# Kernel tuning notes

Measured on AMD Instinct MI355X. Metric: run time of the kernel, lower is better.

## Reference

```python
import jax, jax.numpy as jnp
import numpy as np
import math

SCALES = [1, 2, 4, 8]
H = 1024           # hidden_size
NS = len(SCALES)
DS = H // NS       # per-scale dim = 256
NH_S = max(1, 8 // NS)  # heads per scale = 2


def _avg_pool(x, s):
    # x: [B, L, d], kernel=stride=s (L divisible by s)
    B, L, d = x.shape
    return x.reshape(B, L // s, s, d).mean(axis=2)


def _mha(q, k, v, in_w, in_b, out_w, out_b, nh):
    # torch nn.MultiheadAttention, batch_first, no mask.
    d = q.shape[-1]
    wq, wk, wv = in_w[:d], in_w[d:2 * d], in_w[2 * d:]
    bq, bk, bv = in_b[:d], in_b[d:2 * d], in_b[2 * d:]
    qh = q @ wq.T + bq
    kh = k @ wk.T + bk
    vh = v @ wv.T + bv
    B, Lq, _ = qh.shape
    Lk = kh.shape[1]
    hd = d // nh
    qh = qh.reshape(B, Lq, nh, hd).transpose(0, 2, 1, 3)
    kh = kh.reshape(B, Lk, nh, hd).transpose(0, 2, 1, 3)
    vh = vh.reshape(B, Lk, nh, hd).transpose(0, 2, 1, 3)
    scores = jnp.einsum('bhqd,bhkd->bhqk', qh, kh) * (1.0 / math.sqrt(hd))
    w = jax.nn.softmax(scores, axis=-1)
    out = jnp.einsum('bhqk,bhkd->bhqd', w, vh)
    out = out.transpose(0, 2, 1, 3).reshape(B, Lq, d)
    out = out @ out_w.T + out_b
    return out, w.mean(axis=1)  # averaged attn weights (torch default)


def setup_inputs() -> dict:
    key = jax.random.key(0)
    ks = jax.random.split(key, 20)
    B, S = 4, 2048
    f = lambda k, shape: (jax.random.normal(k, shape, dtype=jnp.float32) * 0.02)
    return {
        'query': jax.random.normal(ks[0], (B, S, H), dtype=jnp.float32),
        'key': jax.random.normal(ks[1], (B, S, H), dtype=jnp.float32),
        'value': jax.random.normal(ks[2], (B, S, H), dtype=jnp.float32),
        'wq': f(ks[3], (H, H)), 'bq': f(ks[4], (H,)),
        'wk': f(ks[5], (H, H)), 'bk': f(ks[6], (H,)),
        'wv': f(ks[7], (H, H)), 'bv': f(ks[8], (H,)),
        'mha_in_w': f(ks[9], (NS, 3 * DS, DS)),
        'mha_in_b': f(ks[10], (NS, 3 * DS)),
        'mha_out_w': f(ks[11], (NS, DS, DS)),
        'mha_out_b': f(ks[12], (NS, DS)),
        'fus_w': f(ks[13], (H, H)), 'fus_b': f(ks[14], (H,)),
    }


def reference(query, key, value, wq, bq, wk, bk, wv, bv,
              mha_in_w, mha_in_b, mha_out_w, mha_out_b, fus_w, fus_b):
    q = query @ wq.T + bq
    k = key @ wk.T + bk
    v = value @ wv.T + bv
    outs = []
    weights0 = None
    for i, s in enumerate(SCALES):
        qs = q[..., i * DS:(i + 1) * DS]
        ks_ = k[..., i * DS:(i + 1) * DS]
        vs = v[..., i * DS:(i + 1) * DS]
        if s > 1:
            ks_ = _avg_pool(ks_, s)
            vs = _avg_pool(vs, s)
        attended, w = _mha(qs, ks_, vs, mha_in_w[i], mha_in_b[i],
                           mha_out_w[i], mha_out_b[i], NH_S)
        # F.interpolate back to seq_len is an identity here (query length == seq_len)
        outs.append(attended)
        if i == 0:
            weights0 = w
    fused = jnp.concatenate(outs, axis=-1) @ fus_w.T + fus_b
    return fused, weights0
```

## Files before the change

### kernel.cpp

```cpp
#include <hip/hip_runtime.h>
#include <stdint.h>

typedef unsigned short u16;
typedef __bf16 v8bf __attribute__((ext_vector_type(8)));
typedef float v4f __attribute__((ext_vector_type(4)));
typedef __attribute__((address_space(3))) unsigned lds_t;
typedef const __attribute__((address_space(1))) unsigned g_t;

__device__ __forceinline__ u16 f2bf(float f) {
  union { float f; unsigned u; } v; v.f = f;
  unsigned r = v.u + 0x7FFFu + ((v.u >> 16) & 1u);
  return (u16)(r >> 16);
}
__device__ __forceinline__ float bf2f(u16 h) {
  union { unsigned u; float f; } v; v.u = ((unsigned)h) << 16;
  return v.f;
}
__device__ __forceinline__ ushort4 f4bf(float4 f) {
  ushort4 o;
  o.x = f2bf(f.x); o.y = f2bf(f.y); o.z = f2bf(f.z); o.w = f2bf(f.w);
  return o;
}
__device__ __forceinline__ long sel4(long4 v, int z) {
  return z == 0 ? v.x : z == 1 ? v.y : z == 2 ? v.z : v.w;
}
__device__ __forceinline__ int sel4i(int4 v, int z) {
  return z == 0 ? v.x : z == 1 ? v.y : z == 2 ? v.z : v.w;
}

__global__ void k_cvt(const float* __restrict__ s, u16* __restrict__ d, long n) {
  long i = ((long)blockIdx.x * blockDim.x + threadIdx.x) * 4;
  long stride = (long)gridDim.x * blockDim.x * 4;
  for (; i < n; i += stride) {
    *(ushort4*)(d + i) = f4bf(*(const float4*)(s + i));
  }
}

__global__ void k_cvtpool(const float* __restrict__ src, u16* __restrict__ dst) {
  int g = blockIdx.x & 255, b = blockIdx.x >> 8;
  int c = threadIdx.x * 4;
  const float* p = src + ((long)b * 2048 + g * 8) * 1024 + c;
  u16* df = dst + ((long)b * 2048 + g * 8) * 1024 + c;
  float4 x[8];
#pragma unroll
  for (int j = 0; j < 8; j++) {
    x[j] = *(const float4*)(p + (long)j * 1024);
    *(ushort4*)(df + (long)j * 1024) = f4bf(x[j]);
  }
  float4 s2[4], s4[2], s8;
#pragma unroll
  for (int j = 0; j < 4; j++) {
    s2[j].x = x[2 * j].x + x[2 * j + 1].x;
    s2[j].y = x[2 * j].y + x[2 * j + 1].y;
    s2[j].z = x[2 * j].z + x[2 * j + 1].z;
    s2[j].w = x[2 * j].w + x[2 * j + 1].w;
  }
#pragma unroll
  for (int j = 0; j < 2; j++) {
    s4[j].x = s2[2 * j].x + s2[2 * j + 1].x;
    s4[j].y = s2[2 * j].y + s2[2 * j + 1].y;
    s4[j].z = s2[2 * j].z + s2[2 * j + 1].z;
    s4[j].w = s2[2 * j].w + s2[2 * j + 1].w;
  }
  s8.x = s4[0].x + s4[1].x; s8.y = s4[0].y + s4[1].y;
  s8.z = s4[0].z + s4[1].z; s8.w = s4[0].w + s4[1].w;
  u16* d2 = dst + ((long)8192 + b * 1024 + g * 4) * 1024 + c;
#pragma unroll
  for (int j = 0; j < 4; j++) {
    float4 t = {s2[j].x * 0.5f, s2[j].y * 0.5f, s2[j].z * 0.5f, s2[j].w * 0.5f};
    *(ushort4*)(d2 + (long)j * 1024) = f4bf(t);
  }
  u16* d4 = dst + ((long)12288 + b * 512 + g * 2) * 1024 + c;
#pragma unroll
  for (int j = 0; j < 2; j++) {
    float4 t = {s4[j].x * 0.25f, s4[j].y * 0.25f, s4[j].z * 0.25f, s4[j].w * 0.25f};
    *(ushort4*)(d4 + (long)j * 1024) = f4bf(t);
  }
  float4 t8 = {s8.x * 0.125f, s8.y * 0.125f, s8.z * 0.125f, s8.w * 0.125f};
  *(ushort4*)(dst + ((long)14336 + b * 256 + g) * 1024 + c) = f4bf(t8);
}

__global__ void k_tc(const float* __restrict__ src, u16* __restrict__ dst, int R, int C) {
  __shared__ float t[32][33];
  long zoff = (long)blockIdx.z * R * C;
  int r0 = blockIdx.y * 32, c0 = blockIdx.x * 32;
  int tx = threadIdx.x & 31, ty = threadIdx.x >> 5;
#pragma unroll
  for (int j = 0; j < 32; j += 8)
    t[ty + j][tx] = src[zoff + (long)(r0 + ty + j) * C + c0 + tx];
  __syncthreads();
#pragma unroll
  for (int j = 0; j < 32; j += 8)
    dst[zoff + (long)(c0 + ty + j) * R + r0 + tx] = f2bf(t[tx][ty + j]);
}

__global__ void k_bcomb_qkv(const float* __restrict__ in_w, const float* __restrict__ in_b,
                            const float* __restrict__ bq, const float* __restrict__ bk,
                            const float* __restrict__ bv, float* __restrict__ out) {
  int gw = (blockIdx.x * 256 + threadIdx.x) >> 6;
  int lane = threadIdx.x & 63;
  int p = gw >> 10, j = gw & 1023, i = j >> 8, of = j & 255;
  const float* bp = p == 0 ? bq : p == 1 ? bk : bv;
  const float* row = in_w + ((long)i * 768 + p * 256 + of) * 256;
  float s = 0.f;
#pragma unroll
  for (int m = 0; m < 4; m++) s += row[lane + m * 64] * bp[i * 256 + lane + m * 64];
#pragma unroll
  for (int m = 32; m >= 1; m >>= 1) s += __shfl_xor(s, m, 64);
  if (lane == 0) out[gw] = in_b[(long)i * 768 + p * 256 + of] + s;
}

__global__ void k_bcomb_f(const float* __restrict__ fw, const float* __restrict__ fb,
                          const float* __restrict__ ob, float* __restrict__ out) {
  int w = (blockIdx.x * 256 + threadIdx.x) >> 6;
  int lane = threadIdx.x & 63;
  const float* row = fw + (long)w * 1024;
  float s = 0.f;
  for (int k = lane; k < 1024; k += 64) s += row[k] * ob[k];
#pragma unroll
  for (int m = 32; m >= 1; m >>= 1) s += __shfl_xor(s, m, 64);
  if (lane == 0) out[w] = fb[w] + s;
}

template<int KS>
__global__ __launch_bounds__(256) void k_ksum(const float* __restrict__ P,
                                              u16* __restrict__ O, long n, int coloff) {
  long i = ((long)blockIdx.x * 256 + threadIdx.x) * 4;
  if (i >= n) return;
  float4 s = *(const float4*)(P + i);
#pragma unroll
  for (int ks = 1; ks < KS; ks++) {
    float4 t = *(const float4*)(P + (long)ks * n + i);
    s.x += t.x; s.y += t.y; s.z += t.z; s.w += t.w;
  }
  *(ushort4*)(O + (i >> 8) * 1024 + coloff + (int)(i & 255)) = f4bf(s);
}

__device__ __forceinline__ float block_allreduce(float x, bool domax) {
  __shared__ float t[4];
  int lane = threadIdx.x & 63, w = threadIdx.x >> 6;
#pragma unroll
  for (int m = 32; m >= 1; m >>= 1) {
    float o = __shfl_xor(x, m, 64);
    x = domax ? fmaxf(x, o) : (x + o);
  }
  __syncthreads();
  if (lane == 0) t[w] = x;
  __syncthreads();
  return domax ? fmaxf(fmaxf(t[0], t[1]), fmaxf(t[2], t[3]))
               : (t[0] + t[1] + t[2] + t[3]);
}

template<int LK>
__global__ __launch_bounds__(256) void k_softmax(u16* __restrict__ P) {
  constexpr int E = LK / 256;
  long row = blockIdx.x;
  u16* p = P + row * (long)LK;
  int tid = threadIdx.x;
  float v[E];
  float mx = -1e30f;
#pragma unroll
  for (int i = 0; i < E; i++) { v[i] = bf2f(p[tid + i * 256]); mx = fmaxf(mx, v[i]); }
  mx = block_allreduce(mx, true);
  float s = 0.f;
#pragma unroll
  for (int i = 0; i < E; i++) { v[i] = __expf(v[i] - mx); s += v[i]; }
  s = block_allreduce(s, false);
  float inv = 1.0f / s;
#pragma unroll
  for (int i = 0; i < E; i++) p[tid + i * 256] = f2bf(v[i] * inv);
}

__global__ __launch_bounds__(256) void k_softmax0(u16* __restrict__ P, float* __restrict__ W0) {
  int bq = blockIdx.x;
  int b = bq >> 11, q = bq & 2047;
  int tid = threadIdx.x;
  float pw[2][8];
  for (int h = 0; h < 2; h++) {
    u16* p = P + (((long)(b * 2 + h) * 2048 + q) * 2048);
    float v[8];
    float mx = -1e30f;
#pragma unroll
    for (int i = 0; i < 8; i++) { v[i] = bf2f(p[tid + i * 256]); mx = fmaxf(mx, v[i]); }
    mx = block_allreduce(mx, true);
    float s = 0.f;
#pragma unroll
    for (int i = 0; i < 8; i++) { v[i] = __expf(v[i] - mx); s += v[i]; }
    s = block_allreduce(s, false);
    float inv = 1.0f / s;
#pragma unroll
    for (int i = 0; i < 8; i++) { pw[h][i] = v[i] * inv; p[tid + i * 256] = f2bf(pw[h][i]); }
  }
  float* wrow = W0 + (long)bq * 2048;
#pragma unroll
  for (int i = 0; i < 8; i++) wrow[tid + i * 256] = 0.5f * (pw[0][i] + pw[1][i]);
}

template<int WBF>
__global__ __launch_bounds__(256) void k_gemm(
    const u16* __restrict__ A, long ldA, long sA1, long sA2,
    const u16* __restrict__ B, long ldB, long sB1, long sB2,
    void* __restrict__ Cv, long ldC, long sC1, long sC2, long sCk,
    const float* __restrict__ bias, long sBias, float alpha,
    int M, int N, int K, int nz2, int KS)
{
  __shared__ u16 As[2][128][32];
  __shared__ u16 Bs[2][128][32];
  int z = blockIdx.z;
  int ks = z % KS; int zz = z / KS;
  int z1 = zz / nz2, z2 = zz - z1 * nz2;
  A += (long)z1 * sA1 + (long)z2 * sA2 + (long)ks * K;
  B += (long)z1 * sB1 + (long)z2 * sB2 + (long)ks * K;
  long coff = (long)z1 * sC1 + (long)z2 * sC2 + (long)ks * sCk;
  const float* bz = bias ? bias + (long)z2 * sBias : nullptr;
  const int m0 = blockIdx.y * 128, n0 = blockIdx.x * 128;
  const int tid = threadIdx.x;
  const int lane = tid & 63;
  const int wave = tid >> 6;
  const int wr = (wave >> 1) * 64, wc = (wave & 1) * 64;
  const int q4 = lane >> 4, l16 = lane & 15;

  const int srow = wave * 16 + (lane >> 2);
  const int scol = (lane & 3) * 8;
  const u16* gA = A + (long)(m0 + srow) * ldA + scol;
  const u16* gB = B + (long)(n0 + srow) * ldB + scol;

  auto stage = [&](int buf, int kt) {
    __builtin_amdgcn_global_load_lds((g_t*)(gA + kt), (lds_t*)&As[buf][wave * 16][0], 16, 0, 0);
    __builtin_amdgcn_global_load_lds((g_t*)(gA + 64 * ldA + kt), (lds_t*)&As[buf][64 + wave * 16][0], 16, 0, 0);
    __builtin_amdgcn_global_load_lds((g_t*)(gB + kt), (lds_t*)&Bs[buf][wave * 16][0], 16, 0, 0);
    __builtin_amdgcn_global_load_lds((g_t*)(gB + 64 * ldB + kt), (lds_t*)&Bs[buf][64 + wave * 16][0], 16, 0, 0);
  };

  v4f acc[4][4];
#pragma unroll
  for (int i = 0; i < 4; i++)
#pragma unroll
    for (int j = 0; j < 4; j++) acc[i][j] = (v4f){0.f, 0.f, 0.f, 0.f};

  stage(0, 0);
  __syncthreads();
  int cur = 0;
  for (int kt = 0; kt < K; kt += 32) {
    if (kt + 32 < K) stage(cur ^ 1, kt + 32);
    v8bf af[4], bf[4];
#pragma unroll
    for (int i = 0; i < 4; i++) af[i] = *(const v8bf*)&As[cur][wr + i * 16 + l16][q4 * 8];
#pragma unroll
    for (int i = 0; i < 4; i++) bf[i] = *(const v8bf*)&Bs[cur][wc + i * 16 + l16][q4 * 8];
#pragma unroll
    for (int mi = 0; mi < 4; mi++)
#pragma unroll
      for (int ni = 0; ni < 4; ni++)
        acc[mi][ni] = __builtin_amdgcn_mfma_f32_16x16x32_bf16(af[mi], bf[ni], acc[mi][ni], 0, 0, 0);
    __syncthreads();
    cur ^= 1;
  }

#pragma unroll
  for (int mi = 0; mi < 4; mi++) {
    int rb = m0 + wr + mi * 16 + q4 * 4;
#pragma unroll
    for (int ni = 0; ni < 4; ni++) {
      int c = n0 + wc + ni * 16 + l16;
      float bv = bz ? bz[c] : 0.f;
#pragma unroll
      for (int i = 0; i < 4; i++) {
        int r = rb + i;
        float val = acc[mi][ni][i] * alpha + bv;
        if (WBF) ((u16*)Cv)[coff + (long)r * ldC + c] = f2bf(val);
        else     ((float*)Cv)[coff + (long)r * ldC + c] = val;
      }
    }
  }
}

template<int TR>
__global__ __launch_bounds__(256) void k_gemm_sm(
    const u16* __restrict__ A, long ldA, long4 aOff,
    const u16* __restrict__ B, long ldB, long sB,
    u16* __restrict__ C, long ldC, long4 cOff,
    const float* __restrict__ bias, long sBias,
    int4 Mz, int K, int4 Lsz)
{
  int z = blockIdx.z;
  int M = sel4i(Mz, z);
  int m0 = blockIdx.y * 128;
  if (m0 >= M) return;
  int n0 = blockIdx.x * 64;
  const u16* Az = A + sel4(aOff, z);
  const u16* Bz = B + (long)z * sB;
  long coff = sel4(cOff, z);
  const float* bz = bias + (long)z * sBias;
  int Ls = sel4i(Lsz, z);
  int lsh = 31 - __clz(Ls);

  __shared__ u16 As[2][128][32];
  __shared__ u16 Bs[2][64][32];
  const int tid = threadIdx.x;
  const int lane = tid & 63, wave = tid >> 6;
  const int q4 = lane >> 4, l16 = lane & 15;
  const int srow = wave * 16 + (lane >> 2);
  const int scol = (lane & 3) * 8;
  const u16* gA = Az + (long)(m0 + srow) * ldA + scol;
  const u16* gB = Bz + (long)(n0 + srow) * ldB + scol;

  auto stage = [&](int buf, int kt) {
    __builtin_amdgcn_global_load_lds((g_t*)(gA + kt), (lds_t*)&As[buf][wave * 16][0], 16, 0, 0);
    __builtin_amdgcn_global_load_lds((g_t*)(gA + 64 * ldA + kt), (lds_t*)&As[buf][64 + wave * 16][0], 16, 0, 0);
    __builtin_amdgcn_global_load_lds((g_t*)(gB + kt), (lds_t*)&Bs[buf][wave * 16][0], 16, 0, 0);
  };

  v4f acc[2][4];
#pragma unroll
  for (int i = 0; i < 2; i++)
#pragma unroll
    for (int j = 0; j < 4; j++) acc[i][j] = (v4f){0.f, 0.f, 0.f, 0.f};

  stage(0, 0);
  __syncthreads();
  int cur = 0;
  for (int kt = 0; kt < K; kt += 32) {
    if (kt + 32 < K) stage(cur ^ 1, kt + 32);
    v8bf af[2], bf[4];
#pragma unroll
    for (int i = 0; i < 2; i++) af[i] = *(const v8bf*)&As[cur][wave * 32 + i * 16 + l16][q4 * 8];
#pragma unroll
    for (int j = 0; j < 4; j++) bf[j] = *(const v8bf*)&Bs[cur][j * 16 + l16][q4 * 8];
#pragma unroll
    for (int mi = 0; mi < 2; mi++)
#pragma unroll
      for (int ni = 0; ni < 4; ni++)
        acc[mi][ni] = __builtin_amdgcn_mfma_f32_16x16x32_bf16(af[mi], bf[ni], acc[mi][ni], 0, 0, 0);
    __syncthreads();
    cur ^= 1;
  }

#pragma unroll
  for (int mi = 0; mi < 2; mi++) {
    int rb = m0 + wave * 32 + mi * 16 + q4 * 4;
#pragma unroll
    for (int ni = 0; ni < 4; ni++) {
      int c = n0 + ni * 16 + l16;
      float bv = bz[c];
#pragma unroll
      for (int i = 0; i < 4; i++) {
        int r = rb + i;
        float val = acc[mi][ni][i] + bv;
        if (TR) {
          int b = r >> lsh, t = r & (Ls - 1);
          int h = c >> 7, n = c & 127;
          C[coff + (((long)(b * 2 + h) * 128 + n) << lsh) + t] = f2bf(val);
        } else {
          C[coff + (long)r * ldC + c] = f2bf(val);
        }
      }
    }
  }
}

extern "C" void kernel_launch(void* const* d_in, const int* in_sizes, int n_in,
                              void* d_out, int out_size, void* d_ws, size_t ws_size,
                              hipStream_t stream) {
  const float* query = (const float*)d_in[0];
  const float* key_  = (const float*)d_in[1];
  const float* value = (const float*)d_in[2];
  const float* wq    = (const float*)d_in[3];
  const float* bq    = (const float*)d_in[4];
  const float* wk    = (const float*)d_in[5];
  const float* bk    = (const float*)d_in[6];
  const float* wv    = (const float*)d_in[7];
  const float* bv    = (const float*)d_in[8];
  const float* in_w  = (const float*)d_in[9];
  const float* in_b  = (const float*)d_in[10];
  const float* out_w = (const float*)d_in[11];
  const float* out_b = (const float*)d_in[12];
  const float* fus_w = (const float*)d_in[13];
  const float* fus_b = (const float*)d_in[14];
  (void)in_sizes; (void)n_in; (void)out_size; (void)ws_size;

  float* outF  = (float*)d_out;
  float* outW0 = outF + (long)4 * 2048 * 1024;

  char* base = (char*)d_ws;
  size_t off = 0;
  auto alloc = [&](size_t bytes) -> void* {
    void* p = base + off;
    off = (off + bytes + 255) & ~(size_t)255;
    return p;
  };
  const long NX = (long)8192 * 1024;
  u16* Winb = (u16*)alloc((size_t)4 * 768 * 256 * 2);
  u16* Wfb  = (u16*)alloc((size_t)1024 * 1024 * 2);
  u16* WoT  = (u16*)alloc((size_t)4 * 256 * 256 * 2);
  u16* WT   = (u16*)alloc((size_t)3 * 1024 * 1024 * 2);
  u16* WC   = (u16*)alloc((size_t)3 * 1024 * 1024 * 2);
  u16* WFc  = (u16*)alloc((size_t)1024 * 1024 * 2);
  float* Bc  = (float*)alloc((size_t)3 * 1024 * 4);
  float* fbc = (float*)alloc((size_t)1024 * 4);
  char* regX = (char*)alloc((size_t)(8192 + 2 * 15360) * 1024 * 2);
  u16* Xq    = (u16*)regX;
  u16* XkAll = Xq + NX;
  u16* XvAll = XkAll + (long)15360 * 1024;
  u16* SC    = (u16*)regX;
  u16* QHf = (u16*)alloc((size_t)8192 * 1024 * 2);
  u16* KH  = (u16*)alloc((size_t)15360 * 256 * 2);
  u16* VHT = (u16*)alloc((size_t)15360 * 256 * 2);
  float* PP = (float*)alloc((size_t)4 * 8192 * 256 * 4);
  u16* AOf = (u16*)alloc((size_t)8192 * 1024 * 2);

  const long rOff[4] = {0, 8192, 12288, 14336};
  const long AOsz = (long)8192 * 256;

  k_cvt<<<1024, 256, 0, stream>>>(query, Xq, NX);
  k_cvtpool<<<1024, 256, 0, stream>>>(key_,  XkAll);
  k_cvtpool<<<1024, 256, 0, stream>>>(value, XvAll);
  k_cvt<<<192, 256, 0, stream>>>(in_w, Winb, 4 * 768 * 256);
  k_cvt<<<256, 256, 0, stream>>>(fus_w, Wfb, 1024 * 1024);
  k_tc<<<dim3(32, 32, 1), 256, 0, stream>>>(wq, WT, 1024, 1024);
  k_tc<<<dim3(32, 32, 1), 256, 0, stream>>>(wk, WT + (long)1024 * 1024, 1024, 1024);
  k_tc<<<dim3(32, 32, 1), 256, 0, stream>>>(wv, WT + (long)2 * 1024 * 1024, 1024, 1024);
  k_tc<<<dim3(8, 8, 4), 256, 0, stream>>>(out_w, WoT, 256, 256);
  k_bcomb_qkv<<<768, 256, 0, stream>>>(in_w, in_b, bq, bk, bv, Bc);
  k_bcomb_f<<<256, 256, 0, stream>>>(fus_w, fus_b, out_b, fbc);

  k_gemm<1><<<dim3(8, 2, 12), 256, 0, stream>>>(
      Winb, 256, 65536, 196608,
      WT, 1024, 1048576, 256,
      WC, 1024, 1048576, 262144, 0,
      nullptr, 0, 1.f, 256, 1024, 256, 4, 1);
  k_gemm<1><<<dim3(2, 8, 4), 256, 0, stream>>>(
      Wfb, 1024, 0, 256,
      WoT, 256, 0, 65536,
      WFc, 1024, 0, 256, 0,
      nullptr, 0, 1.f, 1024, 256, 256, 4, 1);

  k_gemm<1><<<dim3(8, 64, 1), 256, 0, stream>>>(
      Xq, 1024, 0, 0, WC, 1024, 0, 0,
      QHf, 1024, 0, 0, 0, Bc, 0, 1.f, 8192, 1024, 1024, 1, 1);
  {
    long4 aK = {0, (long)8192 * 1024, (long)12288 * 1024, (long)14336 * 1024};
    long4 cK = {0, (long)8192 * 256, (long)12288 * 256, (long)14336 * 256};
    int4  mP = {8192, 4096, 2048, 1024};
    int4  ls1 = {1, 1, 1, 1};
    int4  lsv = {2048, 1024, 512, 256};
    k_gemm_sm<0><<<dim3(4, 64, 4), 256, 0, stream>>>(
        XkAll, 1024, aK, WC + (long)1024 * 1024, 1024, 262144,
        KH, 256, cK, Bc + 1024, 256, mP, 1024, ls1);
    k_gemm_sm<1><<<dim3(4, 64, 4), 256, 0, stream>>>(
        XvAll, 1024, aK, WC + (long)2 * 1024 * 1024, 1024, 262144,
        VHT, 0, cK, Bc + 2048, 256, mP, 1024, lsv);
  }

  const int ksArr[4] = {4, 4, 2, 2};
  for (int i = 0; i < 4; i++) {
    int Lk = 2048 >> i;
    k_gemm<1><<<dim3(Lk / 128, 16, 8), 256, 0, stream>>>(
        QHf + (long)i * 256, 1024, (long)2048 * 1024, 128,
        KH + rOff[i] * 256, 256, (long)Lk * 256, 128,
        SC, Lk, (long)2 * 2048 * Lk, (long)2048 * Lk, 0,
        nullptr, 0, 0.08838834764831845f, 2048, Lk, 128, 2, 1);
    if (i == 0)      k_softmax0<<<8192, 256, 0, stream>>>(SC, outW0);
    else if (i == 1) k_softmax<1024><<<16384, 256, 0, stream>>>(SC);
    else if (i == 2) k_softmax<512><<<16384, 256, 0, stream>>>(SC);
    else             k_softmax<256><<<16384, 256, 0, stream>>>(SC);
    int KS = ksArr[i], Kper = Lk / KS;
    k_gemm<0><<<dim3(1, 16, 8 * KS), 256, 0, stream>>>(
        SC, Lk, (long)2 * 2048 * Lk, (long)2048 * Lk,
        VHT + rOff[i] * 256, Lk, (long)2 * 128 * Lk, (long)128 * Lk,
        PP, 256, (long)2048 * 256, 128, AOsz,
        nullptr, 0, 1.f, 2048, 128, Kper, 2, KS);
    if (KS == 4) k_ksum<4><<<2048, 256, 0, stream>>>(PP, AOf, AOsz, i * 256);
    else         k_ksum<2><<<2048, 256, 0, stream>>>(PP, AOf, AOsz, i * 256);
  }

  k_gemm<0><<<dim3(8, 64, 1), 256, 0, stream>>>(
      AOf, 1024, 0, 0, WFc, 1024, 0, 0,
      outF, 1024, 0, 0, 0, fbc, 0, 1.f, 8192, 1024, 1024, 1, 1);
}
```

Before: 632.3 us.

## Fuse pooled-scale attention into a single flash-attention kernel

Scales 1-3 no longer go through separate score GEMM, softmax, PV GEMM with split-K and a k-sum reduction. One flash-style kernel now handles all three scales, using an online softmax in registers and LDS, staging K and V with global_load_lds, and writing bf16 output straight into AOf. Scale 0 keeps the materialized path because its averaged attention weights must be output. This removes several launches and the global round trips of the score matrix. The trade-off is a single 64-query tile per block with many barriers per K tile, and uneven work per block across scales.

```diff
diff --git a/kernel.cpp b/kernel.cpp
--- a/kernel.cpp
+++ b/kernel.cpp
@@ -151,26 +151,6 @@
                : (t[0] + t[1] + t[2] + t[3]);
 }
 
-template<int LK>
-__global__ __launch_bounds__(256) void k_softmax(u16* __restrict__ P) {
-  constexpr int E = LK / 256;
-  long row = blockIdx.x;
-  u16* p = P + row * (long)LK;
-  int tid = threadIdx.x;
-  float v[E];
-  float mx = -1e30f;
-#pragma unroll
-  for (int i = 0; i < E; i++) { v[i] = bf2f(p[tid + i * 256]); mx = fmaxf(mx, v[i]); }
-  mx = block_allreduce(mx, true);
-  float s = 0.f;
-#pragma unroll
-  for (int i = 0; i < E; i++) { v[i] = __expf(v[i] - mx); s += v[i]; }
-  s = block_allreduce(s, false);
-  float inv = 1.0f / s;
-#pragma unroll
-  for (int i = 0; i < E; i++) p[tid + i * 256] = f2bf(v[i] * inv);
-}
-
 __global__ __launch_bounds__(256) void k_softmax0(u16* __restrict__ P, float* __restrict__ W0) {
   int bq = blockIdx.x;
   int b = bq >> 11, q = bq & 2047;
@@ -194,6 +174,211 @@
   float* wrow = W0 + (long)bq * 2048;
 #pragma unroll
   for (int i = 0; i < 8; i++) wrow[tid + i * 256] = 0.5f * (pw[0][i] + pw[1][i]);
+}
+
+__global__ __launch_bounds__(256) void k_flash(
+    const u16* __restrict__ QHf, const u16* __restrict__ KH,
+    const u16* __restrict__ VHT, u16* __restrict__ AOf)
+{
+  int z = blockIdx.z;
+  int i = (z >> 3) + 1;
+  int b = (z >> 1) & 3, h = z & 1;
+  int Ls = 2048 >> i;
+  int nkt = Ls >> 7;
+  long ro = (long)(16384 - (8192 >> (i - 1))) * 256;
+  int q0 = blockIdx.y * 64;
+
+  __shared__ u16 QP[64][136];
+  __shared__ u16 KV[2][128][32];
+  __shared__ float red[2][4][64];
+
+  const int tid = threadIdx.x, lane = tid & 63, wave = tid >> 6;
+  const int q4 = lane >> 4, l16 = lane & 15;
+  const int wr = (wave >> 1) * 32, wc = (wave & 1) * 64;
+  const int srow = wave * 16 + (lane >> 2);
+  const int scol = (lane & 3) * 8;
+
+  {
+    const u16* gq = QHf + ((long)b * 2048 + q0) * 1024 + i * 256 + h * 128;
+    int idx = tid * 4;
+#pragma unroll
+    for (int j = 0; j < 4; j++) {
+      int r = (idx + j) >> 4, ch = (idx + j) & 15;
+      *(ulonglong2*)&QP[r][ch * 8] = *(const ulonglong2*)(gq + (long)r * 1024 + ch * 8);
+    }
+  }
+  __syncthreads();
+  v8bf qf[2][4];
+#pragma unroll
+  for (int mi = 0; mi < 2; mi++)
+#pragma unroll
+    for (int sub = 0; sub < 4; sub++)
+      qf[mi][sub] = *(const v8bf*)&QP[wr + mi * 16 + l16][sub * 32 + q4 * 8];
+  __syncthreads();
+
+  const u16* gK = KH + ro + (long)b * Ls * 256 + h * 128;
+  const u16* gV = VHT + ro + (long)(b * 2 + h) * 128 * Ls;
+
+  auto stageK = [&](int buf, int kt, int sub) {
+    const u16* g = gK + (long)(kt * 128 + srow) * 256 + sub * 32 + scol;
+    __builtin_amdgcn_global_load_lds((g_t*)g, (lds_t*)&KV[buf][wave * 16][0], 16, 0, 0);
+    __builtin_amdgcn_global_load_lds((g_t*)(g + 64 * 256), (lds_t*)&KV[buf][64 + wave * 16][0], 16, 0, 0);
+  };
+  auto stageV = [&](int buf, int kt, int sub) {
+    const u16* g = gV + (long)srow * Ls + kt * 128 + sub * 32 + scol;
+    __builtin_amdgcn_global_load_lds((g_t*)g, (lds_t*)&KV[buf][wave * 16][0], 16, 0, 0);
+    __builtin_amdgcn_global_load_lds((g_t*)(g + (long)64 * Ls), (lds_t*)&KV[buf][64 + wave * 16][0], 16, 0, 0);
+  };
+
+  v4f acc_o[2][4];
+  float m_run[2][4], l_run[2][4];
+#pragma unroll
+  for (int mi = 0; mi < 2; mi++)
+#pragma unroll
+    for (int ni = 0; ni < 4; ni++) acc_o[mi][ni] = (v4f){0.f, 0.f, 0.f, 0.f};
+#pragma unroll
+  for (int mi = 0; mi < 2; mi++)
+#pragma unroll
+    for (int i4 = 0; i4 < 4; i4++) { m_run[mi][i4] = -1e30f; l_run[mi][i4] = 0.f; }
+
+  const float alpha = 0.08838834764831845f;
+
+  for (int kt = 0; kt < nkt; kt++) {
+    v4f s[2][4];
+#pragma unroll
+    for (int mi = 0; mi < 2; mi++)
+#pragma unroll
+      for (int ni = 0; ni < 4; ni++) s[mi][ni] = (v4f){0.f, 0.f, 0.f, 0.f};
+    stageK(0, kt, 0);
+    __syncthreads();
+    int cur = 0;
+#pragma unroll
+    for (int sub = 0; sub < 4; sub++) {
+      if (sub < 3) stageK(cur ^ 1, kt, sub + 1);
+      v8bf kf[4];
+#pragma unroll
+      for (int ni = 0; ni < 4; ni++)
+        kf[ni] = *(const v8bf*)&KV[cur][wc + ni * 16 + l16][q4 * 8];
+#pragma unroll
+      for (int mi = 0; mi < 2; mi++)
+#pragma unroll
+        for (int ni = 0; ni < 4; ni++)
+          s[mi][ni] = __builtin_amdgcn_mfma_f32_16x16x32_bf16(qf[mi][sub], kf[ni], s[mi][ni], 0, 0, 0);
+      __syncthreads();
+      cur ^= 1;
+    }
+    stageV(0, kt, 0);
+
+#pragma unroll
+    for (int mi = 0; mi < 2; mi++)
+#pragma unroll
+      for (int ni = 0; ni < 4; ni++) s[mi][ni] *= alpha;
+    float mloc[2][4];
+#pragma unroll
+    for (int mi = 0; mi < 2; mi++)
+#pragma unroll
+      for (int i4 = 0; i4 < 4; i4++)
+        mloc[mi][i4] = fmaxf(fmaxf(s[mi][0][i4], s[mi][1][i4]),
+                             fmaxf(s[mi][2][i4], s[mi][3][i4]));
+#pragma unroll
+    for (int d = 1; d <= 8; d <<= 1)
+#pragma unroll
+      for (int mi = 0; mi < 2; mi++)
+#pragma unroll
+        for (int i4 = 0; i4 < 4; i4++)
+          mloc[mi][i4] = fmaxf(mloc[mi][i4], __shfl_xor(mloc[mi][i4], d, 64));
+    if (l16 == 0) {
+#pragma unroll
+      for (int mi = 0; mi < 2; mi++)
+#pragma unroll
+        for (int i4 = 0; i4 < 4; i4++)
+          red[0][wave][wr + mi * 16 + q4 * 4 + i4] = mloc[mi][i4];
+    }
+    __syncthreads();
+    float scl[2][4];
+#pragma unroll
+    for (int mi = 0; mi < 2; mi++)
+#pragma unroll
+      for (int i4 = 0; i4 < 4; i4++) {
+        int rr = wr + mi * 16 + q4 * 4 + i4;
+        float mn = fmaxf(fmaxf(red[0][wave][rr], red[0][wave ^ 1][rr]), m_run[mi][i4]);
+        scl[mi][i4] = __expf(m_run[mi][i4] - mn);
+        m_run[mi][i4] = mn;
+      }
+    float lloc[2][4] = {{0.f, 0.f, 0.f, 0.f}, {0.f, 0.f, 0.f, 0.f}};
+#pragma unroll
+    for (int mi = 0; mi < 2; mi++)
+#pragma unroll
+      for (int ni = 0; ni < 4; ni++)
+#pragma unroll
+        for (int i4 = 0; i4 < 4; i4++) {
+          float p = __expf(s[mi][ni][i4] - m_run[mi][i4]);
+          lloc[mi][i4] += p;
+          QP[wr + mi * 16 + q4 * 4 + i4][wc + ni * 16 + l16] = f2bf(p);
+        }
+#pragma unroll
+    for (int d = 1; d <= 8; d <<= 1)
+#pragma unroll
+      for (int mi = 0; mi < 2; mi++)
+#pragma unroll
+        for (int i4 = 0; i4 < 4; i4++)
+          lloc[mi][i4] += __shfl_xor(lloc[mi][i4], d, 64);
+    if (l16 == 0) {
+#pragma unroll
+      for (int mi = 0; mi < 2; mi++)
+#pragma unroll
+        for (int i4 = 0; i4 < 4; i4++)
+          red[1][wave][wr + mi * 16 + q4 * 4 + i4] = lloc[mi][i4];
+    }
+#pragma unroll
+    for (int mi = 0; mi < 2; mi++)
+#pragma unroll
+      for (int ni = 0; ni < 4; ni++)
+#pragma unroll
+        for (int i4 = 0; i4 < 4; i4++) acc_o[mi][ni][i4] *= scl[mi][i4];
+    __syncthreads();
+#pragma unroll
+    for (int mi = 0; mi < 2; mi++)
+#pragma unroll
+      for (int i4 = 0; i4 < 4; i4++) {
+        int rr = wr + mi * 16 + q4 * 4 + i4;
+        l_run[mi][i4] = l_run[mi][i4] * scl[mi][i4] + red[1][wave][rr] + red[1][wave ^ 1][rr];
+      }
+
+    int cv = 0;
+#pragma unroll
+    for (int sub = 0; sub < 4; sub++) {
+      if (sub < 3) stageV(cv ^ 1, kt, sub + 1);
+      v8bf pf[2], vf[4];
+#pragma unroll
+      for (int mi = 0; mi < 2; mi++)
+        pf[mi] = *(const v8bf*)&QP[wr + mi * 16 + l16][sub * 32 + q4 * 8];
+#pragma unroll
+      for (int ni = 0; ni < 4; ni++)
+        vf[ni] = *(const v8bf*)&KV[cv][wc + ni * 16 + l16][q4 * 8];
+#pragma unroll
+      for (int mi = 0; mi < 2; mi++)
+#pragma unroll
+        for (int ni = 0; ni < 4; ni++)
+          acc_o[mi][ni] = __builtin_amdgcn_mfma_f32_16x16x32_bf16(pf[mi], vf[ni], acc_o[mi][ni], 0, 0, 0);
+      __syncthreads();
+      cv ^= 1;
+    }
+  }
+
+#pragma unroll
+  for (int mi = 0; mi < 2; mi++)
+#pragma unroll
+    for (int i4 = 0; i4 < 4; i4++) {
+      float inv = 1.0f / l_run[mi][i4];
+#pragma unroll
+      for (int ni = 0; ni < 4; ni++) {
+        int r = q0 + wr + mi * 16 + q4 * 4 + i4;
+        int c = wc + ni * 16 + l16;
+        AOf[((long)b * 2048 + r) * 1024 + i * 256 + h * 128 + c] =
+            f2bf(acc_o[mi][ni][i4] * inv);
+      }
+    }
 }
 
 template<int WBF>
@@ -409,7 +594,6 @@
   float* PP = (float*)alloc((size_t)4 * 8192 * 256 * 4);
   u16* AOf = (u16*)alloc((size_t)8192 * 1024 * 2);
 
-  const long rOff[4] = {0, 8192, 12288, 14336};
   const long AOsz = (long)8192 * 256;
 
   k_cvt<<<1024, 256, 0, stream>>>(query, Xq, NX);
@@ -452,27 +636,22 @@
         VHT, 0, cK, Bc + 2048, 256, mP, 1024, lsv);
   }
 
-  const int ksArr[4] = {4, 4, 2, 2};
-  for (int i = 0; i < 4; i++) {
-    int Lk = 2048 >> i;
-    k_gemm<1><<<dim3(Lk / 128, 16, 8), 256, 0, stream>>>(
-        QHf + (long)i * 256, 1024, (long)2048 * 1024, 128,
-        KH + rOff[i] * 256, 256, (long)Lk * 256, 128,
-        SC, Lk, (long)2 * 2048 * Lk, (long)2048 * Lk, 0,
-        nullptr, 0, 0.08838834764831845f, 2048, Lk, 128, 2, 1);
-    if (i == 0)      k_softmax0<<<8192, 256, 0, stream>>>(SC, outW0);
-    else if (i == 1) k_softmax<1024><<<16384, 256, 0, stream>>>(SC);
-    else if (i == 2) k_softmax<512><<<16384, 256, 0, stream>>>(SC);
-    else             k_softmax<256><<<16384, 256, 0, stream>>>(SC);
-    int KS = ksArr[i], Kper = Lk / KS;
-    k_gemm<0><<<dim3(1, 16, 8 * KS), 256, 0, stream>>>(
-        SC, Lk, (long)2 * 2048 * Lk, (long)2048 * Lk,
-        VHT + rOff[i] * 256, Lk, (long)2 * 128 * Lk, (long)128 * Lk,
+  {
+    k_gemm<1><<<dim3(16, 16, 8), 256, 0, stream>>>(
+        QHf, 1024, (long)2048 * 1024, 128,
+        KH, 256, (long)2048 * 256, 128,
+        SC, 2048, (long)2 * 2048 * 2048, (long)2048 * 2048, 0,
+        nullptr, 0, 0.08838834764831845f, 2048, 2048, 128, 2, 1);
+    k_softmax0<<<8192, 256, 0, stream>>>(SC, outW0);
+    k_gemm<0><<<dim3(1, 16, 32), 256, 0, stream>>>(
+        SC, 2048, (long)2 * 2048 * 2048, (long)2048 * 2048,
+        VHT, 2048, (long)2 * 128 * 2048, (long)128 * 2048,
         PP, 256, (long)2048 * 256, 128, AOsz,
-        nullptr, 0, 1.f, 2048, 128, Kper, 2, KS);
-    if (KS == 4) k_ksum<4><<<2048, 256, 0, stream>>>(PP, AOf, AOsz, i * 256);
-    else         k_ksum<2><<<2048, 256, 0, stream>>>(PP, AOf, AOsz, i * 256);
-  }
+        nullptr, 0, 1.f, 2048, 128, 512, 2, 4);
+    k_ksum<4><<<2048, 256, 0, stream>>>(PP, AOf, AOsz, 0);
+  }
+
+  k_flash<<<dim3(1, 32, 24), 256, 0, stream>>>(QHf, KH, VHT, AOf);
 
   k_gemm<0><<<dim3(8, 64, 1), 256, 0, stream>>>(
       AOf, 1024, 0, 0, WFc, 1024, 0, 0,
```

After: 532.2 us. 1.19x faster.
